# Kernel optimization log

Measured on AMD Instinct MI355X. Metric: run time of the kernel, lower is better.

Reference implementation:

```python
import jax, jax.numpy as jnp
import numpy as np

N = 100000      # nodes
E = 1600000     # edges
G = 64          # graphs in batch
H = 128         # hidden (== num_features)
L = 4           # num_layers
C = 16          # num_classes
NCAND = 100000  # candidate edges
BN_EPS = 1e-5


def setup_inputs() -> dict:
    key = jax.random.key(0)
    ks = jax.random.split(key, 24)
    s = 0.05
    inp = {}
    inp["x"] = jax.random.normal(ks[0], (N, H), dtype=jnp.float32)
    inp["edge_index"] = jax.random.randint(ks[1], (2, E), 0, N)
    inp["batch"] = jnp.sort(jax.random.randint(ks[2], (N,), 0, G))
    inp["candidate_edges"] = jax.random.randint(ks[3], (2, NCAND), 0, N)
    # GIN conv params, stacked over L layers (all layers are H->H since num_features==hidden)
    inp["cW1"] = jax.random.normal(ks[4], (L, H, H), dtype=jnp.float32) * s
    inp["cb1"] = jnp.zeros((L, H), jnp.float32)
    inp["cW2"] = jax.random.normal(ks[5], (L, H, H), dtype=jnp.float32) * s
    inp["cb2"] = jnp.zeros((L, H), jnp.float32)
    inp["cgamma"] = jnp.ones((L, H), jnp.float32)
    inp["cbeta"] = jnp.zeros((L, H), jnp.float32)
    inp["ceps"] = jnp.zeros((L,), jnp.float32)  # train_eps=True, init 0
    # node classifier: L*H -> 2H -> H -> H -> C (dropout is identity in eval)
    inp["ncW1"] = jax.random.normal(ks[6], (L * H, 2 * H), dtype=jnp.float32) * s
    inp["ncb1"] = jnp.zeros((2 * H,), jnp.float32)
    inp["ncW2"] = jax.random.normal(ks[7], (2 * H, H), dtype=jnp.float32) * s
    inp["ncb2"] = jnp.zeros((H,), jnp.float32)
    inp["ncW3"] = jax.random.normal(ks[8], (H, H), dtype=jnp.float32) * s
    inp["ncb3"] = jnp.zeros((H,), jnp.float32)
    inp["ncW4"] = jax.random.normal(ks[9], (H, C), dtype=jnp.float32) * s
    inp["ncb4"] = jnp.zeros((C,), jnp.float32)
    # edge predictor: 2*L*H -> 2H -> H -> 1
    inp["epW1"] = jax.random.normal(ks[10], (2 * L * H, 2 * H), dtype=jnp.float32) * s
    inp["epb1"] = jnp.zeros((2 * H,), jnp.float32)
    inp["epW2"] = jax.random.normal(ks[11], (2 * H, H), dtype=jnp.float32) * s
    inp["epb2"] = jnp.zeros((H,), jnp.float32)
    inp["epW3"] = jax.random.normal(ks[12], (H, 1), dtype=jnp.float32) * s
    inp["epb3"] = jnp.zeros((1,), jnp.float32)
    return inp


def _forward(x, cW1, cb1, cW2, cb2, cgamma, cbeta, ceps,
             ncW1, ncb1, ncW2, ncb2, ncW3, ncb3, ncW4, ncb4,
             epW1, epb1, epW2, epb2, epW3, epb3,
             edge_index, batch, candidate_edges):
    src, dst = edge_index[0], edge_index[1]
    h = x
    xs = []
    for l in range(L):
        # GIN: (1+eps)*x_i + sum_{j->i} x_j  (scatter-add over destination nodes)
        agg = jax.ops.segment_sum(h[src], dst, num_segments=N)
        z = (1.0 + ceps[l]) * h + agg
        z = jax.nn.relu(z @ cW1[l] + cb1[l])
        z = jax.nn.relu(z @ cW2[l] + cb2[l])
        # BatchNorm1d (training-mode batch statistics, biased variance)
        mu = z.mean(axis=0)
        var = jnp.var(z, axis=0)
        h = (z - mu) * jax.lax.rsqrt(var + BN_EPS) * cgamma[l] + cbeta[l]
        xs.append(h)
    emb = jnp.concatenate(xs, axis=-1)  # [N, L*H]
    # global mean pool over graphs
    sums = jax.ops.segment_sum(emb, batch, num_segments=G)
    cnt = jax.ops.segment_sum(jnp.ones((N, 1), emb.dtype), batch, num_segments=G)
    gemb = sums / jnp.maximum(cnt, 1.0)  # [G, L*H]
    t = jax.nn.relu(gemb @ ncW1 + ncb1)
    t = jax.nn.relu(t @ ncW2 + ncb2)
    t = jax.nn.relu(t @ ncW3 + ncb3)
    class_output = jax.nn.log_softmax(t @ ncW4 + ncb4, axis=1)  # [G, C]
    # link prediction: gather node embeddings per candidate edge
    ef = jnp.concatenate([emb[candidate_edges[0]], emb[candidate_edges[1]]], axis=1)  # [NC, 2*L*H]
    u = jax.nn.relu(ef @ epW1 + epb1)
    u = jax.nn.relu(u @ epW2 + epb2)
    edge_scores = jax.nn.sigmoid((u @ epW3 + epb3).squeeze(-1))  # [NC]
    return class_output, edge_scores


def reference(x, cW1, cb1, cW2, cb2, cgamma, cbeta, ceps,
              ncW1, ncb1, ncW2, ncb2, ncW3, ncb3, ncW4, ncb4,
              epW1, epb1, epW2, epb2, epW3, epb3,
              edge_index, batch, candidate_edges):
    return _forward(x, cW1, cb1, cW2, cb2, cgamma, cbeta, ceps,
                    ncW1, ncb1, ncW2, ncb2, ncW3, ncb3, ncW4, ncb4,
                    epW1, epb1, epW2, epb2, epW3, epb3,
                    edge_index, batch, candidate_edges)
```

## Files before the change

### kernel.cpp

```cpp
#include <hip/hip_runtime.h>
#include <math.h>

#define NN 100000
#define EE 1600000
#define GG 64
#define HH 128
#define LL 4
#define CCLS 16
#define NC 100000
#define NB 49
#define LDK 40
#define LDA2 136

typedef __attribute__((ext_vector_type(8))) short bf16x8;
typedef __attribute__((ext_vector_type(4))) float f32x4;

__device__ __forceinline__ unsigned short f2bf(float x) {
  union { float f; unsigned int u; } v; v.f = x;
  unsigned int r = v.u + 0x7fffu + ((v.u >> 16) & 1u);
  return (unsigned short)(r >> 16);
}
__device__ __forceinline__ float bl(unsigned u) {
  union { unsigned u; float f; } v; v.u = u << 16; return v.f;
}
__device__ __forceinline__ float bh(unsigned u) {
  union { unsigned u; float f; } v; v.u = u & 0xffff0000u; return v.f;
}

__global__ void hist_kernel(const int* __restrict__ dst, int* __restrict__ cnt, int E) {
  int e = blockIdx.x * 256 + threadIdx.x;
  if (e < E) atomicAdd(&cnt[dst[e]], 1);
}

__global__ __launch_bounds__(256) void scan_p1(const int* __restrict__ cnt,
                                               int* __restrict__ bsum, int n) {
  __shared__ int red[256];
  int tid = threadIdx.x;
  int base = blockIdx.x * 1024 + tid * 4;
  int s = 0;
  if (base + 3 < n) {
    int4 v = *(const int4*)(cnt + base);
    s = v.x + v.y + v.z + v.w;
  } else {
    for (int i = 0; i < 4; ++i) if (base + i < n) s += cnt[base + i];
  }
  red[tid] = s;
  __syncthreads();
  for (int st = 128; st >= 1; st >>= 1) {
    if (tid < st) red[tid] += red[tid + st];
    __syncthreads();
  }
  if (tid == 0) bsum[blockIdx.x] = red[0];
}

__global__ void scan_p2(int* __restrict__ bsum, int* __restrict__ rowptr,
                        int* __restrict__ bcursor, int nb, int n) {
  __shared__ int buf[128];
  int tid = threadIdx.x;
  int v = (tid < nb) ? bsum[tid] : 0;
  buf[tid] = v;
  __syncthreads();
  for (int off = 1; off < 128; off <<= 1) {
    int t = (tid >= off) ? buf[tid - off] : 0;
    __syncthreads();
    buf[tid] += t;
    __syncthreads();
  }
  if (tid < nb) bsum[tid] = buf[tid] - v;
  if (tid == 127) rowptr[n] = buf[127];
  __syncthreads();
  if (tid < NB) bcursor[tid] = (2 * tid < nb) ? (buf[2 * tid] - ((2 * tid < nb) ? bsum[2 * tid] + 0 : 0)) : 0;
  if (tid < NB) bcursor[tid] = bsum[2 * tid];
}

__global__ __launch_bounds__(256) void scan_p3(const int* __restrict__ cnt,
                                               const int* __restrict__ bsum,
                                               int* __restrict__ rowptr,
                                               int* __restrict__ cursor, int n) {
  __shared__ int red[256];
  int tid = threadIdx.x;
  int base = blockIdx.x * 1024 + tid * 4;
  int v[4] = {0, 0, 0, 0};
  if (base + 3 < n) {
    int4 t = *(const int4*)(cnt + base);
    v[0] = t.x; v[1] = t.y; v[2] = t.z; v[3] = t.w;
  } else {
    for (int i = 0; i < 4; ++i) if (base + i < n) v[i] = cnt[base + i];
  }
  int s = v[0] + v[1] + v[2] + v[3];
  red[tid] = s;
  __syncthreads();
  for (int off = 1; off < 256; off <<= 1) {
    int t = (tid >= off) ? red[tid - off] : 0;
    __syncthreads();
    red[tid] += t;
    __syncthreads();
  }
  int run = bsum[blockIdx.x] + red[tid] - s;
  int4 o;
  o.x = run; o.y = run + v[0]; o.z = o.y + v[1]; o.w = o.z + v[2];
  if (base + 3 < n) {
    *(int4*)(rowptr + base) = o;
    *(int4*)(cursor + base) = o;
  } else {
    int oo[4] = {o.x, o.y, o.z, o.w};
    for (int i = 0; i < 4; ++i)
      if (base + i < n) { rowptr[base + i] = oo[i]; cursor[base + i] = oo[i]; }
  }
}

__global__ __launch_bounds__(256) void partition_kernel(const int* __restrict__ src,
                                                        const int* __restrict__ dst,
                                                        int* __restrict__ bcursor,
                                                        int2* __restrict__ pairs, int E) {
  __shared__ int sS[4096];
  __shared__ int sD[4096];
  __shared__ int hist[NB];
  __shared__ int base[NB];
  int tid = threadIdx.x;
  int base_e = blockIdx.x * 4096;
  int cnt = min(4096, E - base_e);
  if (tid < NB) hist[tid] = 0;
  for (int i = tid * 4; i < cnt; i += 1024) {
    if (i + 3 < cnt) {
      *(int4*)(sS + i) = *(const int4*)(src + base_e + i);
      *(int4*)(sD + i) = *(const int4*)(dst + base_e + i);
    } else {
      for (int k = i; k < cnt; ++k) { sS[k] = src[base_e + k]; sD[k] = dst[base_e + k]; }
    }
  }
  __syncthreads();
  for (int i = tid; i < cnt; i += 256) atomicAdd(&hist[sD[i] >> 11], 1);
  __syncthreads();
  if (tid < NB) {
    base[tid] = atomicAdd(&bcursor[tid], hist[tid]);
    hist[tid] = 0;
  }
  __syncthreads();
  for (int i = tid; i < cnt; i += 256) {
    int d = sD[i];
    int b = d >> 11;
    int off = atomicAdd(&hist[b], 1);
    pairs[base[b] + off] = make_int2(sS[i], d);
  }
}

__global__ __launch_bounds__(256) void scatter_csr(const int2* __restrict__ pairs,
                                                   const int* __restrict__ rowptr,
                                                   int* __restrict__ cursor,
                                                   int* __restrict__ csr_src) {
  int b = blockIdx.x % 56;
  int slice = blockIdx.x / 56;
  if (b >= NB) return;
  int start = rowptr[b * 2048];
  int endn = min((b + 1) * 2048, NN);
  int end = rowptr[endn];
  for (int i = start + slice * 256 + threadIdx.x; i < end; i += 8 * 256) {
    int2 p = pairs[i];
    int pos = atomicAdd(&cursor[p.y], 1);
    csr_src[pos] = p.x;
  }
}

__global__ void f2b4_kernel(const float* __restrict__ in, unsigned short* __restrict__ out, int n4) {
  int i = blockIdx.x * 256 + threadIdx.x;
  if (i >= n4) return;
  float4 v = ((const float4*)in)[i];
  unsigned short r[4] = {f2bf(v.x), f2bf(v.y), f2bf(v.z), f2bf(v.w)};
  *(uint2*)(out + (size_t)i * 4) = *(uint2*)r;
}

__global__ void convert_trunk(const float* __restrict__ cW1, const float* __restrict__ cW2,
                              unsigned short* __restrict__ WT1, unsigned short* __restrict__ WT2) {
  int idx = blockIdx.x * 256 + threadIdx.x;
  if (idx >= LL * 16384) return;
  int l = idx >> 14, r = idx & 16383, k = r >> 7, n = r & 127;
  WT1[l * 16384 + n * 128 + k] = f2bf(cW1[idx]);
  WT2[l * 16384 + n * 128 + k] = f2bf(cW2[idx]);
}

__global__ void f2bT_kernel(const float* __restrict__ in, unsigned short* __restrict__ out,
                            int K, int Nn) {
  int idx = blockIdx.x * 256 + threadIdx.x;
  if (idx >= K * Nn) return;
  int k = idx / Nn, n = idx - k * Nn;
  out[(size_t)n * K + k] = f2bf(in[idx]);
}

__global__ void aggregate_bf16(const unsigned short* __restrict__ h16, int ld,
                               const int* __restrict__ rowptr,
                               const int* __restrict__ csr_src,
                               const float* __restrict__ ceps_l,
                               unsigned short* __restrict__ out, int n) {
  int wave = threadIdx.x >> 6;
  int lane = threadIdx.x & 63;
  int sub = lane >> 4;
  int li = lane & 15;
  int node = blockIdx.x * 16 + wave * 4 + sub;
  if (node >= n) return;
  int c8 = li * 8;
  float eps1 = 1.0f + *ceps_l;
  float acc[8] = {};
  int b = rowptr[node], e = rowptr[node + 1];
  int j = b;
  for (; j + 8 <= e; j += 8) {
    uint4 u[8];
#pragma unroll
    for (int t = 0; t < 8; ++t) {
      int s = csr_src[j + t];
      u[t] = *(const uint4*)(h16 + (size_t)s * ld + c8);
    }
#pragma unroll
    for (int t = 0; t < 8; ++t) {
      acc[0] += bl(u[t].x); acc[1] += bh(u[t].x);
      acc[2] += bl(u[t].y); acc[3] += bh(u[t].y);
      acc[4] += bl(u[t].z); acc[5] += bh(u[t].z);
      acc[6] += bl(u[t].w); acc[7] += bh(u[t].w);
    }
  }
  for (; j < e; ++j) {
    int s = csr_src[j];
    uint4 u = *(const uint4*)(h16 + (size_t)s * ld + c8);
    acc[0] += bl(u.x); acc[1] += bh(u.x);
    acc[2] += bl(u.y); acc[3] += bh(u.y);
    acc[4] += bl(u.z); acc[5] += bh(u.z);
    acc[6] += bl(u.w); acc[7] += bh(u.w);
  }
  uint4 hu = *(const uint4*)(h16 + (size_t)node * ld + c8);
  acc[0] = fmaf(eps1, bl(hu.x), acc[0]); acc[1] = fmaf(eps1, bh(hu.x), acc[1]);
  acc[2] = fmaf(eps1, bl(hu.y), acc[2]); acc[3] = fmaf(eps1, bh(hu.y), acc[3]);
  acc[4] = fmaf(eps1, bl(hu.z), acc[4]); acc[5] = fmaf(eps1, bh(hu.z), acc[5]);
  acc[6] = fmaf(eps1, bl(hu.w), acc[6]); acc[7] = fmaf(eps1, bh(hu.w), acc[7]);
  unsigned short o[8];
#pragma unroll
  for (int i = 0; i < 8; ++i) o[i] = f2bf(acc[i]);
  *(uint4*)(out + (size_t)node * 128 + c8) = *(uint4*)o;
}

__global__ __launch_bounds__(256) void trunk_fused(
    const unsigned short* __restrict__ A16,
    const unsigned short* __restrict__ W1T, const float* __restrict__ b1,
    const unsigned short* __restrict__ W2T, const float* __restrict__ b2,
    float* __restrict__ bnsum, float* __restrict__ bnsumsq,
    unsigned short* __restrict__ C16, int M) {
  __shared__ unsigned short As[128 * LDA2];
  __shared__ unsigned short Bs[128 * LDK];
  const int tid = threadIdx.x;
  const int bm = blockIdx.x * 128;
  const int lane = tid & 63;
  const int wave = tid >> 6;
  const int wr = (wave >> 1) << 6;
  const int wc = (wave & 1) << 6;
  const int ar = tid >> 1;
  const int ah = (tid & 1) << 4;
  int gra = bm + ar; if (gra >= M) gra = M - 1;
  const unsigned short* Arow = A16 + (size_t)gra * 128;
  const int mrow = lane & 15;
  const int kq = (lane >> 4) << 3;
  f32x4 acc[4][4] = {};

#pragma unroll
  for (int ks = 0; ks < 4; ++ks) {
    const int k0 = ks << 5;
    const uint4* s = (const uint4*)(Arow + k0 + ah);
    *(uint4*)(As + ar * LDA2 + k0 + ah) = s[0];
    *(uint4*)(As + ar * LDA2 + k0 + ah + 8) = s[1];
  }
  uint4 p0 = *(const uint4*)(W1T + (size_t)ar * 128 + ah);
  uint4 p1 = *(const uint4*)(W1T + (size_t)ar * 128 + ah + 8);
  for (int ks = 0; ks < 4; ++ks) {
    const int k0 = ks << 5;
    *(uint4*)(Bs + ar * LDK + ah) = p0;
    *(uint4*)(Bs + ar * LDK + ah + 8) = p1;
    __syncthreads();
    if (ks < 3) {
      p0 = *(const uint4*)(W1T + (size_t)ar * 128 + k0 + 32 + ah);
      p1 = *(const uint4*)(W1T + (size_t)ar * 128 + k0 + 32 + ah + 8);
    }
    bf16x8 af[4], bfv[4];
#pragma unroll
    for (int t = 0; t < 4; ++t)
      af[t] = *(const bf16x8*)(As + (wr + t * 16 + mrow) * LDA2 + k0 + kq);
#pragma unroll
    for (int t = 0; t < 4; ++t)
      bfv[t] = *(const bf16x8*)(Bs + (wc + t * 16 + mrow) * LDK + kq);
#pragma unroll
    for (int mt = 0; mt < 4; ++mt)
#pragma unroll
      for (int nt = 0; nt < 4; ++nt)
        acc[mt][nt] = __builtin_amdgcn_mfma_f32_16x16x32_bf16(af[mt], bfv[nt], acc[mt][nt], 0, 0, 0);
    __syncthreads();
  }
  const int crow = (lane >> 4) << 2;
  const int ccol = lane & 15;
#pragma unroll
  for (int nt = 0; nt < 4; ++nt) {
    int c = wc + nt * 16 + ccol;
    float bz = b1[c];
#pragma unroll
    for (int mt = 0; mt < 4; ++mt) {
      int rl = wr + mt * 16 + crow;
#pragma unroll
      for (int i = 0; i < 4; ++i)
        As[(rl + i) * LDA2 + c] = f2bf(fmaxf(acc[mt][nt][i] + bz, 0.f));
    }
  }
#pragma unroll
  for (int mt = 0; mt < 4; ++mt)
#pragma unroll
    for (int nt = 0; nt < 4; ++nt)
      acc[mt][nt] = (f32x4){0.f, 0.f, 0.f, 0.f};
  p0 = *(const uint4*)(W2T + (size_t)ar * 128 + ah);
  p1 = *(const uint4*)(W2T + (size_t)ar * 128 + ah + 8);
  __syncthreads();
  for (int ks = 0; ks < 4; ++ks) {
    const int k0 = ks << 5;
    *(uint4*)(Bs + ar * LDK + ah) = p0;
    *(uint4*)(Bs + ar * LDK + ah + 8) = p1;
    __syncthreads();
    if (ks < 3) {
      p0 = *(const uint4*)(W2T + (size_t)ar * 128 + k0 + 32 + ah);
      p1 = *(const uint4*)(W2T + (size_t)ar * 128 + k0 + 32 + ah + 8);
    }
    bf16x8 af[4], bfv[4];
#pragma unroll
    for (int t = 0; t < 4; ++t)
      af[t] = *(const bf16x8*)(As + (wr + t * 16 + mrow) * LDA2 + k0 + kq);
#pragma unroll
    for (int t = 0; t < 4; ++t)
      bfv[t] = *(const bf16x8*)(Bs + (wc + t * 16 + mrow) * LDK + kq);
#pragma unroll
    for (int mt = 0; mt < 4; ++mt)
#pragma unroll
      for (int nt = 0; nt < 4; ++nt)
        acc[mt][nt] = __builtin_amdgcn_mfma_f32_16x16x32_bf16(af[mt], bfv[nt], acc[mt][nt], 0, 0, 0);
    __syncthreads();
  }
#pragma unroll
  for (int nt = 0; nt < 4; ++nt) {
    int c = wc + nt * 16 + ccol;
    float bz = b2[c];
    float s = 0.f, q = 0.f;
#pragma unroll
    for (int mt = 0; mt < 4; ++mt) {
      int rbase = bm + wr + mt * 16 + crow;
#pragma unroll
      for (int i = 0; i < 4; ++i) {
        int r = rbase + i;
        if (r < M) {
          float v = fmaxf(acc[mt][nt][i] + bz, 0.f);
          C16[(size_t)r * 128 + c] = f2bf(v);
          s += v; q += v * v;
        }
      }
    }
    s += __shfl_xor(s, 16, 64);
    s += __shfl_xor(s, 32, 64);
    q += __shfl_xor(q, 16, 64);
    q += __shfl_xor(q, 32, 64);
    if (lane < 16) {
      atomicAdd(&bnsum[c], s);
      atomicAdd(&bnsumsq[c], q);
    }
  }
}

__global__ __launch_bounds__(256) void mfma_gemm_bt(
    const unsigned short* __restrict__ A16, int lda,
    const unsigned short* __restrict__ WT, int K,
    const float* __restrict__ bias,
    unsigned short* __restrict__ C16, int ldc, int M) {
  __shared__ unsigned short As[2][128 * LDK];
  __shared__ unsigned short Bs[2][128 * LDK];
  const int tid = threadIdx.x;
  const int bm = blockIdx.x * 128;
  const int bn = blockIdx.y * 128;
  const int lane = tid & 63;
  const int wave = tid >> 6;
  const int wr = (wave >> 1) << 6;
  const int wc = (wave & 1) << 6;
  f32x4 acc[4][4] = {};
  const int ar = tid >> 1;
  const int ah = (tid & 1) << 4;
  int gra = bm + ar; if (gra >= M) gra = M - 1;
  const unsigned short* Arow = A16 + (size_t)gra * lda;
  const unsigned short* Brow = WT + (size_t)(bn + ar) * K;
  const int mrow = lane & 15;
  const int kq = (lane >> 4) << 3;
  const int nks = K >> 5;

  {
    uint4 a0 = *(const uint4*)(Arow + ah);
    uint4 a1 = *(const uint4*)(Arow + ah + 8);
    uint4 b0 = *(const uint4*)(Brow + ah);
    uint4 b1 = *(const uint4*)(Brow + ah + 8);
    *(uint4*)(As[0] + ar * LDK + ah) = a0;
    *(uint4*)(As[0] + ar * LDK + ah + 8) = a1;
    *(uint4*)(Bs[0] + ar * LDK + ah) = b0;
    *(uint4*)(Bs[0] + ar * LDK + ah + 8) = b1;
  }
  __syncthreads();
  for (int ks = 0; ks < nks; ++ks) {
    const int cur = ks & 1, nxt = cur ^ 1;
    uint4 a0, a1, b0, b1;
    if (ks + 1 < nks) {
      const int k1 = (ks + 1) << 5;
      a0 = *(const uint4*)(Arow + k1 + ah);
      a1 = *(const uint4*)(Arow + k1 + ah + 8);
      b0 = *(const uint4*)(Brow + k1 + ah);
      b1 = *(const uint4*)(Brow + k1 + ah + 8);
    }
    bf16x8 af[4], bfv[4];
#pragma unroll
    for (int t = 0; t < 4; ++t)
      af[t] = *(const bf16x8*)(As[cur] + (wr + t * 16 + mrow) * LDK + kq);
#pragma unroll
    for (int t = 0; t < 4; ++t)
      bfv[t] = *(const bf16x8*)(Bs[cur] + (wc + t * 16 + mrow) * LDK + kq);
#pragma unroll
    for (int mt = 0; mt < 4; ++mt)
#pragma unroll
      for (int nt = 0; nt < 4; ++nt)
        acc[mt][nt] = __builtin_amdgcn_mfma_f32_16x16x32_bf16(af[mt], bfv[nt], acc[mt][nt], 0, 0, 0);
    if (ks + 1 < nks) {
      *(uint4*)(As[nxt] + ar * LDK + ah) = a0;
      *(uint4*)(As[nxt] + ar * LDK + ah + 8) = a1;
      *(uint4*)(Bs[nxt] + ar * LDK + ah) = b0;
      *(uint4*)(Bs[nxt] + ar * LDK + ah + 8) = b1;
      __syncthreads();
    }
  }
  const int crow = (lane >> 4) << 2;
  const int ccol = lane & 15;
#pragma unroll
  for (int nt = 0; nt < 4; ++nt) {
    int cbase = bn + wc + nt * 16 + ccol;
    float bz = bias[cbase];
#pragma unroll
    for (int mt = 0; mt < 4; ++mt) {
      int rbase = bm + wr + mt * 16 + crow;
#pragma unroll
      for (int i = 0; i < 4; ++i) {
        int r = rbase + i;
        if (r < M) C16[(size_t)r * ldc + cbase] = f2bf(fmaxf(acc[mt][nt][i] + bz, 0.f));
      }
    }
  }
}

__global__ __launch_bounds__(512) void mfma_gemm_gather(
    const unsigned short* __restrict__ emb16, const int* __restrict__ cand,
    const unsigned short* __restrict__ WT ,
    const float* __restrict__ bias,
    unsigned short* __restrict__ C16 , int M) {
  __shared__ unsigned short As[2][128 * LDK];
  __shared__ unsigned short Bs[2][256 * LDK];
  const int tid = threadIdx.x;
  const int bm = blockIdx.x * 128;
  const int lane = tid & 63;
  const int wave = tid >> 6;
  const int wr = (wave >> 2) << 6;
  const int wc = (wave & 3) << 6;
  f32x4 acc[4][4] = {};
  const int ar = tid >> 2;
  const int ah = (tid & 3) << 3;
  int gra = bm + ar; if (gra >= M) gra = M - 1;
  const int node0 = cand[gra];
  const int node1 = cand[NC + gra];
  const int br = tid >> 1;
  const int bh8 = (tid & 1) << 4;
  const unsigned short* Brow = WT + (size_t)br * 1024 + bh8;
  const int mrow = lane & 15;
  const int kq = (lane >> 4) << 3;

  {
    uint4 a = *(const uint4*)(emb16 + (size_t)node0 * 512 + ah);
    uint4 b0 = *(const uint4*)(Brow);
    uint4 b1 = *(const uint4*)(Brow + 8);
    *(uint4*)(As[0] + ar * LDK + ah) = a;
    *(uint4*)(Bs[0] + br * LDK + bh8) = b0;
    *(uint4*)(Bs[0] + br * LDK + bh8 + 8) = b1;
  }
  __syncthreads();
  for (int ks = 0; ks < 32; ++ks) {
    const int cur = ks & 1, nxt = cur ^ 1;
    uint4 a, b0, b1;
    if (ks < 31) {
      const int k1 = (ks + 1) << 5;
      int node = (k1 < 512) ? node0 : node1;
      a = *(const uint4*)(emb16 + (size_t)node * 512 + (k1 & 511) + ah);
      b0 = *(const uint4*)(Brow + k1);
      b1 = *(const uint4*)(Brow + k1 + 8);
    }
    bf16x8 af[4], bfv[4];
#pragma unroll
    for (int t = 0; t < 4; ++t)
      af[t] = *(const bf16x8*)(As[cur] + (wr + t * 16 + mrow) * LDK + kq);
#pragma unroll
    for (int t = 0; t < 4; ++t)
      bfv[t] = *(const bf16x8*)(Bs[cur] + (wc + t * 16 + mrow) * LDK + kq);
#pragma unroll
    for (int mt = 0; mt < 4; ++mt)
#pragma unroll
      for (int nt = 0; nt < 4; ++nt)
        acc[mt][nt] = __builtin_amdgcn_mfma_f32_16x16x32_bf16(af[mt], bfv[nt], acc[mt][nt], 0, 0, 0);
    if (ks < 31) {
      *(uint4*)(As[nxt] + ar * LDK + ah) = a;
      *(uint4*)(Bs[nxt] + br * LDK + bh8) = b0;
      *(uint4*)(Bs[nxt] + br * LDK + bh8 + 8) = b1;
      __syncthreads();
    }
  }
  const int crow = (lane >> 4) << 2;
  const int ccol = lane & 15;
#pragma unroll
  for (int nt = 0; nt < 4; ++nt) {
    int cbase = wc + nt * 16 + ccol;
    float bz = bias[cbase];
#pragma unroll
    for (int mt = 0; mt < 4; ++mt) {
      int rbase = bm + wr + mt * 16 + crow;
#pragma unroll
      for (int i = 0; i < 4; ++i) {
        int r = rbase + i;
        if (r < M) C16[(size_t)r * 256 + cbase] = f2bf(fmaxf(acc[mt][nt][i] + bz, 0.f));
      }
    }
  }
}

__global__ void bn_apply_bf16(const unsigned short* __restrict__ z,
                              const float* __restrict__ sum, const float* __restrict__ sumsq,
                              const float* __restrict__ gamma, const float* __restrict__ beta,
                              unsigned short* __restrict__ out, int n) {
  int idx = blockIdx.x * 256 + threadIdx.x;
  if (idx >= n * 16) return;
  int r = idx >> 4, c8 = (idx & 15) << 3;
  uint4 v = *(const uint4*)(z + (size_t)r * 128 + c8);
  float f[8] = {bl(v.x), bh(v.x), bl(v.y), bh(v.y), bl(v.z), bh(v.z), bl(v.w), bh(v.w)};
  const float inv_n = 1.0f / (float)NN;
  unsigned short o[8];
#pragma unroll
  for (int j = 0; j < 8; ++j) {
    int c = c8 + j;
    float mu = sum[c] * inv_n;
    float var = sumsq[c] * inv_n - mu * mu;
    float sc = rsqrtf(var + 1e-5f) * gamma[c];
    o[j] = f2bf((f[j] - mu) * sc + beta[c]);
  }
  *(uint4*)(out + (size_t)r * 512 + c8) = *(uint4*)o;
}

__global__ void bounds_kernel(const int* __restrict__ batch, int* __restrict__ gstart, int n) {
  int g = threadIdx.x;
  if (g > GG) return;
  int lo = 0, hi = n;
  while (lo < hi) {
    int mid = (lo + hi) >> 1;
    if (batch[mid] < g) lo = mid + 1; else hi = mid;
  }
  gstart[g] = lo;
}

__global__ __launch_bounds__(256) void pool_bf16(const unsigned short* __restrict__ emb16,
                                                 const int* __restrict__ gstart,
                                                 float* __restrict__ gsum) {
  int g = blockIdx.x;
  int chunk = blockIdx.y;
  int c2 = threadIdx.x * 2;
  int s = gstart[g], e = gstart[g + 1];
  int len = e - s;
  int per = (len + 7) >> 3;
  int r0 = s + chunk * per;
  int r1 = min(r0 + per, e);
  float ax = 0.f, ay = 0.f;
  for (int r = r0; r < r1; ++r) {
    unsigned u = *(const unsigned*)(emb16 + (size_t)r * 512 + c2);
    ax += bl(u); ay += bh(u);
  }
  if (r1 > r0) {
    atomicAdd(&gsum[g * 512 + c2], ax);
    atomicAdd(&gsum[g * 512 + c2 + 1], ay);
  }
}

__global__ __launch_bounds__(256) void nc_fused(
    const float* __restrict__ gsum, const int* __restrict__ gstart,
    const float* __restrict__ W1, const float* __restrict__ b1,
    const float* __restrict__ W2, const float* __restrict__ b2,
    const float* __restrict__ W3, const float* __restrict__ b3,
    const float* __restrict__ W4, const float* __restrict__ b4,
    float* __restrict__ out) {
  __shared__ float row[512];
  __shared__ float t1[256];
  __shared__ float t2[128];
  __shared__ float t3s[128];
  __shared__ float lg[16];
  int g = blockIdx.x;
  int tid = threadIdx.x;
  float inv = 1.0f / fmaxf((float)(gstart[g + 1] - gstart[g]), 1.0f);
  row[tid] = gsum[g * 512 + tid] * inv;
  row[tid + 256] = gsum[g * 512 + tid + 256] * inv;
  __syncthreads();
  {
    float acc = b1[tid];
#pragma unroll 8
    for (int k = 0; k < 512; ++k) acc = fmaf(row[k], W1[k * 256 + tid], acc);
    t1[tid] = fmaxf(acc, 0.f);
  }
  __syncthreads();
  if (tid < 128) {
    float acc = b2[tid];
#pragma unroll 8
    for (int k = 0; k < 256; ++k) acc = fmaf(t1[k], W2[k * 128 + tid], acc);
    t2[tid] = fmaxf(acc, 0.f);
  }
  __syncthreads();
  if (tid < 128) {
    float acc = b3[tid];
#pragma unroll 8
    for (int k = 0; k < 128; ++k) acc = fmaf(t2[k], W3[k * 128 + tid], acc);
    t3s[tid] = fmaxf(acc, 0.f);
  }
  __syncthreads();
  if (tid < 16) {
    float acc = b4[tid];
#pragma unroll 8
    for (int k = 0; k < 128; ++k) acc = fmaf(t3s[k], W4[k * 16 + tid], acc);
    lg[tid] = acc;
  }
  __syncthreads();
  if (tid < 16) {
    float v = lg[tid];
    float m = v;
    for (int j = 0; j < 16; ++j) m = fmaxf(m, lg[j]);
    float s = 0.f;
    for (int j = 0; j < 16; ++j) s += expf(lg[j] - m);
    out[g * 16 + tid] = v - m - logf(s);
  }
}

__global__ void ep_final_bf16(const unsigned short* __restrict__ C2, const float* __restrict__ w,
                              const float* __restrict__ b3, float* __restrict__ out, int M) {
  int row = blockIdx.x * 4 + (threadIdx.x >> 6);
  if (row >= M) return;
  int lane = threadIdx.x & 63;
  int c2 = lane * 2;
  unsigned u = *(const unsigned*)(C2 + (size_t)row * 128 + c2);
  float2 wv = *(const float2*)(w + c2);
  float s = bl(u) * wv.x + bh(u) * wv.y;
  for (int off = 32; off >= 1; off >>= 1) s += __shfl_down(s, off, 64);
  if (lane == 0) out[row] = 1.f / (1.f + expf(-(s + b3[0])));
}

extern "C" void kernel_launch(void* const* d_in, const int* in_sizes, int n_in,
                              void* d_out, int out_size, void* d_ws, size_t ws_size,
                              hipStream_t stream) {
  const float* x = (const float*)d_in[0];
  const int* edge_index = (const int*)d_in[1];
  const int* batch = (const int*)d_in[2];
  const int* cand = (const int*)d_in[3];
  const float* cW1 = (const float*)d_in[4];
  const float* cb1 = (const float*)d_in[5];
  const float* cW2 = (const float*)d_in[6];
  const float* cb2 = (const float*)d_in[7];
  const float* cgamma = (const float*)d_in[8];
  const float* cbeta = (const float*)d_in[9];
  const float* ceps = (const float*)d_in[10];
  const float* ncW1 = (const float*)d_in[11];
  const float* ncb1 = (const float*)d_in[12];
  const float* ncW2 = (const float*)d_in[13];
  const float* ncb2 = (const float*)d_in[14];
  const float* ncW3 = (const float*)d_in[15];
  const float* ncb3 = (const float*)d_in[16];
  const float* ncW4 = (const float*)d_in[17];
  const float* ncb4 = (const float*)d_in[18];
  const float* epW1 = (const float*)d_in[19];
  const float* epb1 = (const float*)d_in[20];
  const float* epW2 = (const float*)d_in[21];
  const float* epb2 = (const float*)d_in[22];
  const float* epW3 = (const float*)d_in[23];
  const float* epb3 = (const float*)d_in[24];

  char* ws = (char*)d_ws;
  size_t off = 0;
  auto alloc = [&](size_t bytes) -> void* {
    off = (off + 255) & ~(size_t)255;
    void* p = ws + off;
    off += bytes;
    return p;
  };
  size_t zz_bytes = (size_t)NN * 4 + 512 * 4 + 512 * 4 + (size_t)GG * 512 * 4;
  char* zz = (char*)alloc(zz_bytes);
  int* cnt = (int*)zz;
  float* bnsum = (float*)(zz + (size_t)NN * 4);
  float* bnsumsq = bnsum + 512;
  float* gsum = bnsumsq + 512;
  int* rowptr = (int*)alloc((size_t)(NN + 1) * 4);
  int* cursor = (int*)alloc((size_t)NN * 4);
  int* csr_src = (int*)alloc((size_t)EE * 4);
  int2* pairs = (int2*)alloc((size_t)EE * 8);
  int* bsum = (int*)alloc(128 * 4);
  int* bcursor = (int*)alloc(64 * 4);
  unsigned short* x16 = (unsigned short*)alloc((size_t)NN * 128 * 2);
  unsigned short* g16a = (unsigned short*)alloc((size_t)NN * 128 * 2);
  unsigned short* emb16 = (unsigned short*)alloc((size_t)NN * 512 * 2);
  unsigned short* C1 = (unsigned short*)alloc((size_t)NC * 256 * 2);
  unsigned short* C2 = (unsigned short*)alloc((size_t)NC * 128 * 2);
  unsigned short* WT1 = (unsigned short*)alloc((size_t)LL * 16384 * 2);
  unsigned short* WT2 = (unsigned short*)alloc((size_t)LL * 16384 * 2);
  unsigned short* W1T = (unsigned short*)alloc((size_t)1024 * 256 * 2);
  unsigned short* W2T = (unsigned short*)alloc((size_t)256 * 128 * 2);
  int* gstart = (int*)alloc(65 * 4);

  const int* esrc = edge_index;
  const int* edst = edge_index + EE;
  const int nblk = (NN + 1023) / 1024;
  const int nech = (EE + 4095) / 4096;

  hipMemsetAsync(zz, 0, zz_bytes, stream);
  hist_kernel<<<(EE + 255) / 256, 256, 0, stream>>>(edst, cnt, EE);
  scan_p1<<<nblk, 256, 0, stream>>>(cnt, bsum, NN);
  scan_p2<<<1, 128, 0, stream>>>(bsum, rowptr, bcursor, nblk, NN);
  scan_p3<<<nblk, 256, 0, stream>>>(cnt, bsum, rowptr, cursor, NN);
  partition_kernel<<<nech, 256, 0, stream>>>(esrc, edst, bcursor, pairs, EE);
  scatter_csr<<<56 * 8, 256, 0, stream>>>(pairs, rowptr, cursor, csr_src);
  f2b4_kernel<<<(NN * 128 / 4 + 255) / 256, 256, 0, stream>>>(x, x16, NN * 128 / 4);
  convert_trunk<<<(LL * 16384 + 255) / 256, 256, 0, stream>>>(cW1, cW2, WT1, WT2);
  f2bT_kernel<<<(1024 * 256 + 255) / 256, 256, 0, stream>>>(epW1, W1T, 1024, 256);
  f2bT_kernel<<<(256 * 128 + 255) / 256, 256, 0, stream>>>(epW2, W2T, 256, 128);

  for (int l = 0; l < LL; ++l) {
    const unsigned short* h16 = (l == 0) ? x16 : (emb16 + (size_t)(l - 1) * 128);
    int ld = (l == 0) ? 128 : 512;
    aggregate_bf16<<<(NN + 15) / 16, 256, 0, stream>>>(h16, ld, rowptr, csr_src, ceps + l, g16a, NN);
    trunk_fused<<<(NN + 127) / 128, 256, 0, stream>>>(
        g16a, WT1 + (size_t)l * 16384, cb1 + l * 128,
        WT2 + (size_t)l * 16384, cb2 + l * 128,
        bnsum + l * 128, bnsumsq + l * 128, g16a, NN);
    bn_apply_bf16<<<(NN * 16 + 255) / 256, 256, 0, stream>>>(
        g16a, bnsum + l * 128, bnsumsq + l * 128, cgamma + l * 128, cbeta + l * 128,
        emb16 + (size_t)l * 128, NN);
  }

  bounds_kernel<<<1, 128, 0, stream>>>(batch, gstart, NN);
  pool_bf16<<<dim3(GG, 8), 256, 0, stream>>>(emb16, gstart, gsum);
  nc_fused<<<GG, 256, 0, stream>>>(gsum, gstart, ncW1, ncb1, ncW2, ncb2, ncW3, ncb3,
                                   ncW4, ncb4, (float*)d_out);

  mfma_gemm_gather<<<(NC + 127) / 128, 512, 0, stream>>>(emb16, cand, W1T, epb1, C1, NC);
  mfma_gemm_bt<<<dim3((NC + 127) / 128, 1), 256, 0, stream>>>(C1, 256, W2T, 256, epb2, C2, 128, NC);
  ep_final_bf16<<<(NC + 3) / 4, 256, 0, stream>>>(C2, epW3, epb3, (float*)d_out + GG * CCLS, NC);
}
```

Baseline: 1.127 ms.

## Bucket candidate edges by source node for gather locality, deepen A prefetch

Adds a three-kernel counting sort that groups candidate edges into buckets by the high bits of their first node index. The edge-predictor gather GEMM then processes rows in that order and scatters results back to the original rows through a shared-memory index table. The aim is better cache locality for the random embedding gathers, and the gathered A tile is now prefetched two k-steps ahead to hide its latency. The three weight-conversion kernels are also merged into one launch; in exchange the change adds three small kernels and scattered output writes.

```diff
diff --git a/kernel.cpp b/kernel.cpp
--- a/kernel.cpp
+++ b/kernel.cpp
@@ -69,7 +69,6 @@
   if (tid < nb) bsum[tid] = buf[tid] - v;
   if (tid == 127) rowptr[n] = buf[127];
   __syncthreads();
-  if (tid < NB) bcursor[tid] = (2 * tid < nb) ? (buf[2 * tid] - ((2 * tid < nb) ? bsum[2 * tid] + 0 : 0)) : 0;
   if (tid < NB) bcursor[tid] = bsum[2 * tid];
 }
 
@@ -162,6 +161,59 @@
   }
 }
 
+__global__ __launch_bounds__(256) void cand_hist(const int* __restrict__ cand,
+                                                 int* __restrict__ cbkt, int N) {
+  __shared__ int h[NB];
+  int tid = threadIdx.x;
+  if (tid < NB) h[tid] = 0;
+  __syncthreads();
+  int end = min(blockIdx.x * 4096 + 4096, N);
+  for (int i = blockIdx.x * 4096 + tid; i < end; i += 256) atomicAdd(&h[cand[i] >> 11], 1);
+  __syncthreads();
+  if (tid < NB) atomicAdd(&cbkt[tid], h[tid]);
+}
+
+__global__ void cand_scan(const int* __restrict__ cbkt, int* __restrict__ ccur) {
+  __shared__ int buf[64];
+  int tid = threadIdx.x;
+  int v = (tid < NB) ? cbkt[tid] : 0;
+  buf[tid] = v;
+  __syncthreads();
+  for (int off = 1; off < 64; off <<= 1) {
+    int t = (tid >= off) ? buf[tid - off] : 0;
+    __syncthreads();
+    buf[tid] += t;
+    __syncthreads();
+  }
+  if (tid < NB) ccur[tid] = buf[tid] - v;
+}
+
+__global__ __launch_bounds__(256) void cand_part(const int* __restrict__ cand,
+                                                 int* __restrict__ ccur,
+                                                 int* __restrict__ cidx, int N) {
+  __shared__ int sC[4096];
+  __shared__ int h[NB];
+  __shared__ int base[NB];
+  int tid = threadIdx.x;
+  int b0 = blockIdx.x * 4096;
+  int cnt = min(4096, N - b0);
+  if (tid < NB) h[tid] = 0;
+  for (int i = tid; i < cnt; i += 256) sC[i] = cand[b0 + i];
+  __syncthreads();
+  for (int i = tid; i < cnt; i += 256) atomicAdd(&h[sC[i] >> 11], 1);
+  __syncthreads();
+  if (tid < NB) {
+    base[tid] = atomicAdd(&ccur[tid], h[tid]);
+    h[tid] = 0;
+  }
+  __syncthreads();
+  for (int i = tid; i < cnt; i += 256) {
+    int b = sC[i] >> 11;
+    int off = atomicAdd(&h[b], 1);
+    cidx[base[b] + off] = b0 + i;
+  }
+}
+
 __global__ void f2b4_kernel(const float* __restrict__ in, unsigned short* __restrict__ out, int n4) {
   int i = blockIdx.x * 256 + threadIdx.x;
   if (i >= n4) return;
@@ -170,21 +222,24 @@
   *(uint2*)(out + (size_t)i * 4) = *(uint2*)r;
 }
 
-__global__ void convert_trunk(const float* __restrict__ cW1, const float* __restrict__ cW2,
-                              unsigned short* __restrict__ WT1, unsigned short* __restrict__ WT2) {
+__global__ void conv_weights(const float* __restrict__ cW1, const float* __restrict__ cW2,
+                             unsigned short* __restrict__ WT1, unsigned short* __restrict__ WT2,
+                             const float* __restrict__ epW1, unsigned short* __restrict__ W1T,
+                             const float* __restrict__ epW2, unsigned short* __restrict__ W2T) {
   int idx = blockIdx.x * 256 + threadIdx.x;
-  if (idx >= LL * 16384) return;
-  int l = idx >> 14, r = idx & 16383, k = r >> 7, n = r & 127;
-  WT1[l * 16384 + n * 128 + k] = f2bf(cW1[idx]);
-  WT2[l * 16384 + n * 128 + k] = f2bf(cW2[idx]);
-}
-
-__global__ void f2bT_kernel(const float* __restrict__ in, unsigned short* __restrict__ out,
-                            int K, int Nn) {
-  int idx = blockIdx.x * 256 + threadIdx.x;
-  if (idx >= K * Nn) return;
-  int k = idx / Nn, n = idx - k * Nn;
-  out[(size_t)n * K + k] = f2bf(in[idx]);
+  if (idx < LL * 16384) {
+    int l = idx >> 14, r = idx & 16383, k = r >> 7, n = r & 127;
+    WT1[l * 16384 + n * 128 + k] = f2bf(cW1[idx]);
+    WT2[l * 16384 + n * 128 + k] = f2bf(cW2[idx]);
+  } else if (idx < LL * 16384 + 262144) {
+    int j = idx - LL * 16384;
+    int k = j >> 8, n = j & 255;
+    W1T[(size_t)n * 1024 + k] = f2bf(epW1[j]);
+  } else if (idx < LL * 16384 + 262144 + 32768) {
+    int j = idx - LL * 16384 - 262144;
+    int k = j >> 7, n = j & 127;
+    W2T[(size_t)n * 256 + k] = f2bf(epW2[j]);
+  }
 }
 
 __global__ void aggregate_bf16(const unsigned short* __restrict__ h16, int ld,
@@ -450,11 +505,13 @@
 
 __global__ __launch_bounds__(512) void mfma_gemm_gather(
     const unsigned short* __restrict__ emb16, const int* __restrict__ cand,
+    const int* __restrict__ cidx,
     const unsigned short* __restrict__ WT ,
     const float* __restrict__ bias,
     unsigned short* __restrict__ C16 , int M) {
   __shared__ unsigned short As[2][128 * LDK];
   __shared__ unsigned short Bs[2][256 * LDK];
+  __shared__ int sRid[128];
   const int tid = threadIdx.x;
   const int bm = blockIdx.x * 128;
   const int lane = tid & 63;
@@ -465,14 +522,19 @@
   const int ar = tid >> 2;
   const int ah = (tid & 3) << 3;
   int gra = bm + ar; if (gra >= M) gra = M - 1;
-  const int node0 = cand[gra];
-  const int node1 = cand[NC + gra];
+  const int rid = cidx[gra];
+  const int node0 = cand[rid];
+  const int node1 = cand[NC + rid];
   const int br = tid >> 1;
   const int bh8 = (tid & 1) << 4;
   const unsigned short* Brow = WT + (size_t)br * 1024 + bh8;
   const int mrow = lane & 15;
   const int kq = (lane >> 4) << 3;
 
+  if (tid < 128) {
+    int g = bm + tid; if (g >= M) g = M - 1;
+    sRid[tid] = cidx[g];
+  }
   {
     uint4 a = *(const uint4*)(emb16 + (size_t)node0 * 512 + ah);
     uint4 b0 = *(const uint4*)(Brow);
@@ -481,16 +543,20 @@
     *(uint4*)(Bs[0] + br * LDK + bh8) = b0;
     *(uint4*)(Bs[0] + br * LDK + bh8 + 8) = b1;
   }
+  uint4 aP = *(const uint4*)(emb16 + (size_t)node0 * 512 + 32 + ah);
   __syncthreads();
   for (int ks = 0; ks < 32; ++ks) {
     const int cur = ks & 1, nxt = cur ^ 1;
-    uint4 a, b0, b1;
+    uint4 bb0, bb1, aN;
     if (ks < 31) {
       const int k1 = (ks + 1) << 5;
-      int node = (k1 < 512) ? node0 : node1;
-      a = *(const uint4*)(emb16 + (size_t)node * 512 + (k1 & 511) + ah);
-      b0 = *(const uint4*)(Brow + k1);
-      b1 = *(const uint4*)(Brow + k1 + 8);
+      bb0 = *(const uint4*)(Brow + k1);
+      bb1 = *(const uint4*)(Brow + k1 + 8);
+    }
+    if (ks < 30) {
+      const int k2 = (ks + 2) << 5;
+      int node = (k2 < 512) ? node0 : node1;
+      aN = *(const uint4*)(emb16 + (size_t)node * 512 + (k2 & 511) + ah);
     }
     bf16x8 af[4], bfv[4];
 #pragma unroll
@@ -505,9 +571,10 @@
       for (int nt = 0; nt < 4; ++nt)
         acc[mt][nt] = __builtin_amdgcn_mfma_f32_16x16x32_bf16(af[mt], bfv[nt], acc[mt][nt], 0, 0, 0);
     if (ks < 31) {
-      *(uint4*)(As[nxt] + ar * LDK + ah) = a;
-      *(uint4*)(Bs[nxt] + br * LDK + bh8) = b0;
-      *(uint4*)(Bs[nxt] + br * LDK + bh8 + 8) = b1;
+      *(uint4*)(As[nxt] + ar * LDK + ah) = aP;
+      *(uint4*)(Bs[nxt] + br * LDK + bh8) = bb0;
+      *(uint4*)(Bs[nxt] + br * LDK + bh8 + 8) = bb1;
+      aP = aN;
       __syncthreads();
     }
   }
@@ -519,11 +586,14 @@
     float bz = bias[cbase];
 #pragma unroll
     for (int mt = 0; mt < 4; ++mt) {
-      int rbase = bm + wr + mt * 16 + crow;
+      int rel = wr + mt * 16 + crow;
 #pragma unroll
       for (int i = 0; i < 4; ++i) {
-        int r = rbase + i;
-        if (r < M) C16[(size_t)r * 256 + cbase] = f2bf(fmaxf(acc[mt][nt][i] + bz, 0.f));
+        int r = bm + rel + i;
+        if (r < M) {
+          int rr = sRid[rel + i];
+          C16[(size_t)rr * 256 + cbase] = f2bf(fmaxf(acc[mt][nt][i] + bz, 0.f));
+        }
       }
     }
   }
@@ -690,18 +760,21 @@
     off += bytes;
     return p;
   };
-  size_t zz_bytes = (size_t)NN * 4 + 512 * 4 + 512 * 4 + (size_t)GG * 512 * 4;
+  size_t zz_bytes = (size_t)NN * 4 + 512 * 4 + 512 * 4 + (size_t)GG * 512 * 4 + 64 * 4;
   char* zz = (char*)alloc(zz_bytes);
   int* cnt = (int*)zz;
   float* bnsum = (float*)(zz + (size_t)NN * 4);
   float* bnsumsq = bnsum + 512;
   float* gsum = bnsumsq + 512;
+  int* cbkt = (int*)(gsum + (size_t)GG * 512);
   int* rowptr = (int*)alloc((size_t)(NN + 1) * 4);
   int* cursor = (int*)alloc((size_t)NN * 4);
   int* csr_src = (int*)alloc((size_t)EE * 4);
   int2* pairs = (int2*)alloc((size_t)EE * 8);
   int* bsum = (int*)alloc(128 * 4);
   int* bcursor = (int*)alloc(64 * 4);
+  int* ccur = (int*)alloc(64 * 4);
+  int* cidx = (int*)alloc((size_t)NC * 4);
   unsigned short* x16 = (unsigned short*)alloc((size_t)NN * 128 * 2);
   unsigned short* g16a = (unsigned short*)alloc((size_t)NN * 128 * 2);
   unsigned short* emb16 = (unsigned short*)alloc((size_t)NN * 512 * 2);
@@ -717,18 +790,21 @@
   const int* edst = edge_index + EE;
   const int nblk = (NN + 1023) / 1024;
   const int nech = (EE + 4095) / 4096;
+  const int ncch = (NC + 4095) / 4096;
 
   hipMemsetAsync(zz, 0, zz_bytes, stream);
   hist_kernel<<<(EE + 255) / 256, 256, 0, stream>>>(edst, cnt, EE);
+  cand_hist<<<ncch, 256, 0, stream>>>(cand, cbkt, NC);
   scan_p1<<<nblk, 256, 0, stream>>>(cnt, bsum, NN);
   scan_p2<<<1, 128, 0, stream>>>(bsum, rowptr, bcursor, nblk, NN);
   scan_p3<<<nblk, 256, 0, stream>>>(cnt, bsum, rowptr, cursor, NN);
+  cand_scan<<<1, 64, 0, stream>>>(cbkt, ccur);
+  cand_part<<<ncch, 256, 0, stream>>>(cand, ccur, cidx, NC);
   partition_kernel<<<nech, 256, 0, stream>>>(esrc, edst, bcursor, pairs, EE);
   scatter_csr<<<56 * 8, 256, 0, stream>>>(pairs, rowptr, cursor, csr_src);
   f2b4_kernel<<<(NN * 128 / 4 + 255) / 256, 256, 0, stream>>>(x, x16, NN * 128 / 4);
-  convert_trunk<<<(LL * 16384 + 255) / 256, 256, 0, stream>>>(cW1, cW2, WT1, WT2);
-  f2bT_kernel<<<(1024 * 256 + 255) / 256, 256, 0, stream>>>(epW1, W1T, 1024, 256);
-  f2bT_kernel<<<(256 * 128 + 255) / 256, 256, 0, stream>>>(epW2, W2T, 256, 128);
+  conv_weights<<<(LL * 16384 + 262144 + 32768 + 255) / 256, 256, 0, stream>>>(
+      cW1, cW2, WT1, WT2, epW1, W1T, epW2, W2T);
 
   for (int l = 0; l < LL; ++l) {
     const unsigned short* h16 = (l == 0) ? x16 : (emb16 + (size_t)(l - 1) * 128);
@@ -748,7 +824,7 @@
   nc_fused<<<GG, 256, 0, stream>>>(gsum, gstart, ncW1, ncb1, ncW2, ncb2, ncW3, ncb3,
                                    ncW4, ncb4, (float*)d_out);
 
-  mfma_gemm_gather<<<(NC + 127) / 128, 512, 0, stream>>>(emb16, cand, W1T, epb1, C1, NC);
+  mfma_gemm_gather<<<(NC + 127) / 128, 512, 0, stream>>>(emb16, cand, cidx, W1T, epb1, C1, NC);
   mfma_gemm_bt<<<dim3((NC + 127) / 128, 1), 256, 0, stream>>>(C1, 256, W2T, 256, epb2, C2, 128, NC);
   ep_final_bf16<<<(NC + 3) / 4, 256, 0, stream>>>(C2, epW3, epb3, (float*)d_out + GG * CCLS, NC);
 }
```

New measurement: 1.139 ms. No clear change (+1.1%).

## Load edge-predictor GEMM fragments directly from global memory, merge weight conversions

Applied to the files above, without the earlier changes.

The first edge-predictor GEMM no longer stages A and B tiles through double-buffered shared memory with per-step barriers. Each wave now loads its MFMA fragments straight from global memory (gathered embedding rows and transposed weights) into registers, with a one-step register prefetch. The three weight-conversion kernels are merged into one launch, and a redundant store in scan_p2 is dropped. This removes LDS traffic and syncs but gives up cross-wave reuse, so global and L2 load traffic goes up about fourfold.

```diff
diff --git a/kernel.cpp b/kernel.cpp
--- a/kernel.cpp
+++ b/kernel.cpp
@@ -69,7 +69,6 @@
   if (tid < nb) bsum[tid] = buf[tid] - v;
   if (tid == 127) rowptr[n] = buf[127];
   __syncthreads();
-  if (tid < NB) bcursor[tid] = (2 * tid < nb) ? (buf[2 * tid] - ((2 * tid < nb) ? bsum[2 * tid] + 0 : 0)) : 0;
   if (tid < NB) bcursor[tid] = bsum[2 * tid];
 }
 
@@ -170,21 +169,24 @@
   *(uint2*)(out + (size_t)i * 4) = *(uint2*)r;
 }
 
-__global__ void convert_trunk(const float* __restrict__ cW1, const float* __restrict__ cW2,
-                              unsigned short* __restrict__ WT1, unsigned short* __restrict__ WT2) {
+__global__ void conv_weights(const float* __restrict__ cW1, const float* __restrict__ cW2,
+                             unsigned short* __restrict__ WT1, unsigned short* __restrict__ WT2,
+                             const float* __restrict__ epW1, unsigned short* __restrict__ W1T,
+                             const float* __restrict__ epW2, unsigned short* __restrict__ W2T) {
   int idx = blockIdx.x * 256 + threadIdx.x;
-  if (idx >= LL * 16384) return;
-  int l = idx >> 14, r = idx & 16383, k = r >> 7, n = r & 127;
-  WT1[l * 16384 + n * 128 + k] = f2bf(cW1[idx]);
-  WT2[l * 16384 + n * 128 + k] = f2bf(cW2[idx]);
-}
-
-__global__ void f2bT_kernel(const float* __restrict__ in, unsigned short* __restrict__ out,
-                            int K, int Nn) {
-  int idx = blockIdx.x * 256 + threadIdx.x;
-  if (idx >= K * Nn) return;
-  int k = idx / Nn, n = idx - k * Nn;
-  out[(size_t)n * K + k] = f2bf(in[idx]);
+  if (idx < LL * 16384) {
+    int l = idx >> 14, r = idx & 16383, k = r >> 7, n = r & 127;
+    WT1[l * 16384 + n * 128 + k] = f2bf(cW1[idx]);
+    WT2[l * 16384 + n * 128 + k] = f2bf(cW2[idx]);
+  } else if (idx < LL * 16384 + 262144) {
+    int j = idx - LL * 16384;
+    int k = j >> 8, n = j & 255;
+    W1T[(size_t)n * 1024 + k] = f2bf(epW1[j]);
+  } else if (idx < LL * 16384 + 262144 + 32768) {
+    int j = idx - LL * 16384 - 262144;
+    int k = j >> 7, n = j & 127;
+    W2T[(size_t)n * 256 + k] = f2bf(epW2[j]);
+  }
 }
 
 __global__ void aggregate_bf16(const unsigned short* __restrict__ h16, int ld,
@@ -448,68 +450,68 @@
   }
 }
 
-__global__ __launch_bounds__(512) void mfma_gemm_gather(
+__global__ __launch_bounds__(512) void ep_gemm1_stream(
     const unsigned short* __restrict__ emb16, const int* __restrict__ cand,
     const unsigned short* __restrict__ WT ,
     const float* __restrict__ bias,
     unsigned short* __restrict__ C16 , int M) {
-  __shared__ unsigned short As[2][128 * LDK];
-  __shared__ unsigned short Bs[2][256 * LDK];
+  __shared__ int sN0[128];
+  __shared__ int sN1[128];
   const int tid = threadIdx.x;
   const int bm = blockIdx.x * 128;
   const int lane = tid & 63;
   const int wave = tid >> 6;
   const int wr = (wave >> 2) << 6;
   const int wc = (wave & 3) << 6;
-  f32x4 acc[4][4] = {};
-  const int ar = tid >> 2;
-  const int ah = (tid & 3) << 3;
-  int gra = bm + ar; if (gra >= M) gra = M - 1;
-  const int node0 = cand[gra];
-  const int node1 = cand[NC + gra];
-  const int br = tid >> 1;
-  const int bh8 = (tid & 1) << 4;
-  const unsigned short* Brow = WT + (size_t)br * 1024 + bh8;
   const int mrow = lane & 15;
   const int kq = (lane >> 4) << 3;
-
-  {
-    uint4 a = *(const uint4*)(emb16 + (size_t)node0 * 512 + ah);
-    uint4 b0 = *(const uint4*)(Brow);
-    uint4 b1 = *(const uint4*)(Brow + 8);
-    *(uint4*)(As[0] + ar * LDK + ah) = a;
-    *(uint4*)(Bs[0] + br * LDK + bh8) = b0;
-    *(uint4*)(Bs[0] + br * LDK + bh8 + 8) = b1;
-  }
-  __syncthreads();
+  if (tid < 128) {
+    int g = bm + tid; if (g >= M) g = M - 1;
+    sN0[tid] = cand[g];
+    sN1[tid] = cand[NC + g];
+  }
+  __syncthreads();
+  int n0[4], n1[4];
+  const unsigned short* brow[4];
+#pragma unroll
+  for (int mt = 0; mt < 4; ++mt) {
+    int r = wr + mt * 16 + mrow;
+    n0[mt] = sN0[r];
+    n1[mt] = sN1[r];
+  }
+#pragma unroll
+  for (int nt = 0; nt < 4; ++nt)
+    brow[nt] = WT + (size_t)(wc + nt * 16 + mrow) * 1024 + kq;
+  f32x4 acc[4][4] = {};
+  bf16x8 afP[4], bfP[4];
+#pragma unroll
+  for (int mt = 0; mt < 4; ++mt)
+    afP[mt] = *(const bf16x8*)(emb16 + (size_t)n0[mt] * 512 + kq);
+#pragma unroll
+  for (int nt = 0; nt < 4; ++nt)
+    bfP[nt] = *(const bf16x8*)(brow[nt]);
   for (int ks = 0; ks < 32; ++ks) {
-    const int cur = ks & 1, nxt = cur ^ 1;
-    uint4 a, b0, b1;
+    bf16x8 af[4], bf[4];
+#pragma unroll
+    for (int t = 0; t < 4; ++t) { af[t] = afP[t]; bf[t] = bfP[t]; }
     if (ks < 31) {
       const int k1 = (ks + 1) << 5;
-      int node = (k1 < 512) ? node0 : node1;
-      a = *(const uint4*)(emb16 + (size_t)node * 512 + (k1 & 511) + ah);
-      b0 = *(const uint4*)(Brow + k1);
-      b1 = *(const uint4*)(Brow + k1 + 8);
-    }
-    bf16x8 af[4], bfv[4];
-#pragma unroll
-    for (int t = 0; t < 4; ++t)
-      af[t] = *(const bf16x8*)(As[cur] + (wr + t * 16 + mrow) * LDK + kq);
-#pragma unroll
-    for (int t = 0; t < 4; ++t)
-      bfv[t] = *(const bf16x8*)(Bs[cur] + (wc + t * 16 + mrow) * LDK + kq);
+      const int col = (k1 & 511) + kq;
+      const bool first = (k1 < 512);
+#pragma unroll
+      for (int mt = 0; mt < 4; ++mt) {
+        int node = first ? n0[mt] : n1[mt];
+        afP[mt] = *(const bf16x8*)(emb16 + (size_t)node * 512 + col);
+      }
+#pragma unroll
+      for (int nt = 0; nt < 4; ++nt)
+        bfP[nt] = *(const bf16x8*)(brow[nt] + k1);
+    }
 #pragma unroll
     for (int mt = 0; mt < 4; ++mt)
 #pragma unroll
       for (int nt = 0; nt < 4; ++nt)
-        acc[mt][nt] = __builtin_amdgcn_mfma_f32_16x16x32_bf16(af[mt], bfv[nt], acc[mt][nt], 0, 0, 0);
-    if (ks < 31) {
-      *(uint4*)(As[nxt] + ar * LDK + ah) = a;
-      *(uint4*)(Bs[nxt] + br * LDK + bh8) = b0;
-      *(uint4*)(Bs[nxt] + br * LDK + bh8 + 8) = b1;
-      __syncthreads();
-    }
+        acc[mt][nt] = __builtin_amdgcn_mfma_f32_16x16x32_bf16(af[mt], bf[nt], acc[mt][nt], 0, 0, 0);
   }
   const int crow = (lane >> 4) << 2;
   const int ccol = lane & 15;
@@ -726,9 +728,8 @@
   partition_kernel<<<nech, 256, 0, stream>>>(esrc, edst, bcursor, pairs, EE);
   scatter_csr<<<56 * 8, 256, 0, stream>>>(pairs, rowptr, cursor, csr_src);
   f2b4_kernel<<<(NN * 128 / 4 + 255) / 256, 256, 0, stream>>>(x, x16, NN * 128 / 4);
-  convert_trunk<<<(LL * 16384 + 255) / 256, 256, 0, stream>>>(cW1, cW2, WT1, WT2);
-  f2bT_kernel<<<(1024 * 256 + 255) / 256, 256, 0, stream>>>(epW1, W1T, 1024, 256);
-  f2bT_kernel<<<(256 * 128 + 255) / 256, 256, 0, stream>>>(epW2, W2T, 256, 128);
+  conv_weights<<<(LL * 16384 + 262144 + 32768 + 255) / 256, 256, 0, stream>>>(
+      cW1, cW2, WT1, WT2, epW1, W1T, epW2, W2T);
 
   for (int l = 0; l < LL; ++l) {
     const unsigned short* h16 = (l == 0) ? x16 : (emb16 + (size_t)(l - 1) * 128);
@@ -748,7 +749,7 @@
   nc_fused<<<GG, 256, 0, stream>>>(gsum, gstart, ncW1, ncb1, ncW2, ncb2, ncW3, ncb3,
                                    ncW4, ncb4, (float*)d_out);
 
-  mfma_gemm_gather<<<(NC + 127) / 128, 512, 0, stream>>>(emb16, cand, W1T, epb1, C1, NC);
+  ep_gemm1_stream<<<(NC + 127) / 128, 512, 0, stream>>>(emb16, cand, W1T, epb1, C1, NC);
   mfma_gemm_bt<<<dim3((NC + 127) / 128, 1), 256, 0, stream>>>(C1, 256, W2T, 256, epb2, C2, 128, NC);
   ep_final_bf16<<<(NC + 3) / 4, 256, 0, stream>>>(C2, epW3, epb3, (float*)d_out + GG * CCLS, NC);
 }
```

New measurement: 1.285 ms. 14.1% more time.
